# Kernel tuning notes

Measured on AMD Instinct MI355X. Metric: run time of the kernel, lower is better.

Reference implementation:

```python
import jax, jax.numpy as jnp
import numpy as np

DIM = 768
HEADS = 12
HEAD_DIM = DIM // HEADS
SCALE = HEAD_DIM ** (-0.5)


def setup_inputs() -> dict:
    key = jax.random.key(0)
    k1, k2, k3, k4 = jax.random.split(key, 4)
    B, N = 2, 48 * 48
    x = jax.random.normal(k1, (B, N, DIM), dtype=jnp.float32)
    qkv_w = jax.random.normal(k2, (3 * DIM, DIM), dtype=jnp.float32) * (DIM ** -0.5)
    proj_w = jax.random.normal(k3, (DIM, DIM), dtype=jnp.float32) * (DIM ** -0.5)
    proj_b = jax.random.normal(k4, (DIM,), dtype=jnp.float32) * 0.02
    return {"x": x, "H": 48, "W": 48, "qkv_w": qkv_w, "proj_w": proj_w, "proj_b": proj_b}


def reference(x, H, W, qkv_w, proj_w, proj_b):
    B, N, C = x.shape
    h, d = HEADS, HEAD_DIM
    # qkv linear (no bias): [B,N,3C], then split into per-head q,k,v [B,h,N,d]
    qkv = jnp.einsum('bnc,fc->bnf', x, qkv_w)
    qkv = qkv.reshape(B, N, 3, h, d).transpose(2, 0, 3, 1, 4)
    q, k, v = qkv[0], qkv[1], qkv[2]
    attn = jnp.einsum('bhnd,bhmd->bhnm', q, k) * SCALE  # [B,h,N,N]
    attn = jax.nn.softmax(attn, axis=-1)
    out = jnp.einsum('bhnm,bhmd->bhnd', attn, v)  # [B,h,N,d]
    out = out.transpose(0, 2, 1, 3).reshape(B, N, C)
    out = jnp.einsum('bnc,fc->bnf', out, proj_w) + proj_b
    return out
```

## Files before the change

kernel.cpp:

```cpp
#include <hip/hip_runtime.h>

#define B_    2
#define N_    2304
#define C_    768
#define HEADS 12
#define D_    64
#define F3    2304
#define M_    (B_*N_)
#define SPLITS 2
#define KSPAN (N_/SPLITS)
#define QSCALE 0.18033688011112042f

typedef __attribute__((ext_vector_type(8)))  short bfrag;
typedef __attribute__((ext_vector_type(4)))  float ffrag;
typedef __attribute__((ext_vector_type(16))) float ffrag16;

__device__ __forceinline__ short f2bf(float f) {
    unsigned u = __float_as_uint(f);
    u += 0x7fff + ((u >> 16) & 1);
    return (short)(u >> 16);
}

__device__ __forceinline__ void gl2lds16(const void* g, void* l) {
    __builtin_amdgcn_global_load_lds(
        (const __attribute__((address_space(1))) void*)g,
        (__attribute__((address_space(3))) void*)l, 16, 0, 0);
}

__global__ __launch_bounds__(256) void cast_bf16(const float* __restrict__ src,
                                                 short* __restrict__ dst, int n4) {
    int i = blockIdx.x * 256 + threadIdx.x;
    if (i < n4) {
        float4 v = ((const float4*)src)[i];
        short4 o;
        o.x = f2bf(v.x); o.y = f2bf(v.y); o.z = f2bf(v.z); o.w = f2bf(v.w);
        ((short4*)dst)[i] = o;
    }
}

__global__ __launch_bounds__(256) void qkv_gemm(const short* __restrict__ xb,
                                                const short* __restrict__ wb,
                                                short* __restrict__ Qb,
                                                short* __restrict__ Kb,
                                                short* __restrict__ Vtb) {
    __shared__ short As[128*32];
    __shared__ short Bs[128*32];
    const int t = threadIdx.x;
    const int w = t >> 6, lane = t & 63;
    const int quad = lane >> 4, l15 = lane & 15;
    const int wr = w >> 1, wc = w & 1;
    const int m0 = blockIdx.y * 128, f0 = blockIdx.x * 128;

    ffrag acc[4][4] = {};

    for (int k0 = 0; k0 < C_; k0 += 32) {
        __syncthreads();
        #pragma unroll
        for (int r = 0; r < 2; ++r) {
            int seg = r*4 + w;
            int row = seg*16 + (lane >> 2);
            int kk  = (lane & 3) * 8;
            gl2lds16(xb + (size_t)(m0+row)*C_ + k0 + kk, As + seg*512);
            gl2lds16(wb + (size_t)(f0+row)*C_ + k0 + kk, Bs + seg*512);
        }
        __syncthreads();
        bfrag af[4], bf[4];
        #pragma unroll
        for (int i = 0; i < 4; ++i)
            af[i] = *(const bfrag*)(As + (wr*64 + i*16 + l15)*32 + quad*8);
        #pragma unroll
        for (int j = 0; j < 4; ++j)
            bf[j] = *(const bfrag*)(Bs + (wc*64 + j*16 + l15)*32 + quad*8);
        #pragma unroll
        for (int i = 0; i < 4; ++i)
            #pragma unroll
            for (int j = 0; j < 4; ++j)
                acc[i][j] = __builtin_amdgcn_mfma_f32_16x16x32_bf16(af[i], bf[j], acc[i][j], 0, 0, 0);
    }

    const int b   = m0 / N_;
    const int seg = f0 + wc*64;
    const int which = seg / C_;
    const int head  = (seg - which*C_) >> 6;
    const int bh    = b*HEADS + head;
    const int nbase = (m0 - b*N_) + wr*64 + quad*4;

    if (which == 0) {
        #pragma unroll
        for (int i = 0; i < 4; ++i) {
            int n0 = nbase + i*16;
            #pragma unroll
            for (int j = 0; j < 4; ++j) {
                int d = j*16 + l15;
                #pragma unroll
                for (int r = 0; r < 4; ++r)
                    Qb[((size_t)bh*N_ + n0 + r)*D_ + d] = f2bf(acc[i][j][r] * QSCALE);
            }
        }
    } else if (which == 1) {
        #pragma unroll
        for (int i = 0; i < 4; ++i) {
            int n0 = nbase + i*16;
            #pragma unroll
            for (int j = 0; j < 4; ++j) {
                int d = j*16 + l15;
                #pragma unroll
                for (int r = 0; r < 4; ++r)
                    Kb[((size_t)bh*N_ + n0 + r)*D_ + d] = f2bf(acc[i][j][r]);
            }
        }
    } else {
        #pragma unroll
        for (int i = 0; i < 4; ++i) {
            int n0 = nbase + i*16;
            #pragma unroll
            for (int j = 0; j < 4; ++j) {
                int d = j*16 + l15;
                short4 vv;
                vv.x = f2bf(acc[i][j][0]);
                vv.y = f2bf(acc[i][j][1]);
                vv.z = f2bf(acc[i][j][2]);
                vv.w = f2bf(acc[i][j][3]);
                *(short4*)(Vtb + ((size_t)bh*D_ + d)*N_ + n0) = vv;
            }
        }
    }
}

__global__ __launch_bounds__(128) void attn_mfma(const short* __restrict__ Qb,
                                                 const short* __restrict__ Kb,
                                                 const short* __restrict__ Vtb,
                                                 float* __restrict__ Opart,
                                                 float* __restrict__ lpart) {
    __shared__ short PQ[64*72];
    __shared__ short Ks[64*64];
    __shared__ short Vts[64*64];
    const int t = threadIdx.x;
    const int w = t >> 6, lane = t & 63;
    const int l31 = lane & 31, hi = lane >> 5;
    const int bh = blockIdx.x, q0 = blockIdx.y * 64;
    const int split = blockIdx.z;
    const int kbase = split * KSPAN;
    const size_t base = (size_t)bh * N_ * D_;
    const int lrow = lane >> 3;
    const int lc   = (lane & 7) ^ lrow;

    #pragma unroll
    for (int r = 0; r < 4; ++r) {
        int s = r*2 + w;
        int row = s*8 + lrow;
        gl2lds16(Qb + base + (size_t)(q0+row)*D_ + lc*8, PQ + s*512);
    }
    __syncthreads();

    bfrag qf[4];
    {
        int row = w*32 + l31, r7 = row & 7;
        #pragma unroll
        for (int kc = 0; kc < 4; ++kc)
            qf[kc] = *(const bfrag*)(PQ + row*64 + ((kc*2 + hi) ^ r7)*8);
    }

    ffrag16 oacc[2];
    float l_acc[16];
    #pragma unroll
    for (int r = 0; r < 16; ++r) {
        l_acc[r] = 0.f; oacc[0][r] = 0.f; oacc[1][r] = 0.f;
    }

    for (int k0 = kbase; k0 < kbase + KSPAN; k0 += 64) {
        __syncthreads();
        #pragma unroll
        for (int r = 0; r < 4; ++r) {
            int s = r*2 + w;
            int row = s*8 + lrow;
            gl2lds16(Kb  + base + (size_t)(k0+row)*D_ + lc*8,    Ks  + s*512);
            gl2lds16(Vtb + (size_t)(bh*D_ + row)*N_ + k0 + lc*8, Vts + s*512);
        }
        __syncthreads();

        #pragma unroll
        for (int kt = 0; kt < 2; ++kt) {
            ffrag16 s;
            #pragma unroll
            for (int r = 0; r < 16; ++r) s[r] = 0.f;
            int row = kt*32 + l31, r7 = row & 7;
            #pragma unroll
            for (int kc = 0; kc < 4; ++kc) {
                bfrag kf = *(const bfrag*)(Ks + row*64 + ((kc*2 + hi) ^ r7)*8);
                s = __builtin_amdgcn_mfma_f32_32x32x16_bf16(qf[kc], kf, s, 0, 0, 0);
            }
            #pragma unroll
            for (int r = 0; r < 16; ++r) {
                float p = __builtin_amdgcn_exp2f(s[r]);
                l_acc[r] += p;
                int prow = (r & 3) + 8*(r >> 2) + 4*hi;
                PQ[(w*32 + prow)*72 + kt*32 + l31] = f2bf(p);
            }
        }

        #pragma unroll
        for (int kc = 0; kc < 4; ++kc) {
            bfrag pf = *(const bfrag*)(PQ + (w*32 + l31)*72 + kc*16 + hi*8);
            #pragma unroll
            for (int dt = 0; dt < 2; ++dt) {
                int row = dt*32 + l31, r7 = row & 7;
                bfrag vf = *(const bfrag*)(Vts + row*64 + ((kc*2 + hi) ^ r7)*8);
                oacc[dt] = __builtin_amdgcn_mfma_f32_32x32x16_bf16(pf, vf, oacc[dt], 0, 0, 0);
            }
        }
    }

    #pragma unroll
    for (int r = 0; r < 16; ++r) {
        float v = l_acc[r];
        v += __shfl_xor(v, 1, 64);
        v += __shfl_xor(v, 2, 64);
        v += __shfl_xor(v, 4, 64);
        v += __shfl_xor(v, 8, 64);
        v += __shfl_xor(v, 16, 64);
        l_acc[r] = v;
    }

    const int b = bh / HEADS, head = bh - b*HEADS;
    float* Op = Opart + (size_t)split * M_ * C_;
    float* lp = lpart + (size_t)split * (B_*HEADS) * N_;

    if (l31 == 0) {
        #pragma unroll
        for (int r = 0; r < 16; ++r) {
            int n = q0 + w*32 + (r & 3) + 8*(r >> 2) + 4*hi;
            lp[bh*N_ + n] = l_acc[r];
        }
    }
    #pragma unroll
    for (int dt = 0; dt < 2; ++dt)
        #pragma unroll
        for (int r = 0; r < 16; ++r) {
            int n = q0 + w*32 + (r & 3) + 8*(r >> 2) + 4*hi;
            int c = head*D_ + dt*32 + l31;
            Op[((size_t)b*N_ + n)*C_ + c] = oacc[dt][r];
        }
}

__global__ __launch_bounds__(256) void attn_merge(const float* __restrict__ Opart,
                                                  const float* __restrict__ lpart,
                                                  short* __restrict__ Ob) {
    int i = blockIdx.x * 256 + threadIdx.x;
    int m = i / (C_/4);
    int c = (i - m*(C_/4)) * 4;
    int b = m / N_, n = m - b*N_;
    int bh = b*HEADS + (c >> 6);
    float4 o0 = ((const float4*)Opart)[i];
    float4 o1 = ((const float4*)(Opart + (size_t)M_*C_))[i];
    float l = lpart[bh*N_ + n] + lpart[(B_*HEADS)*N_ + bh*N_ + n];
    float inv = 1.f / l;
    short4 o;
    o.x = f2bf((o0.x + o1.x) * inv);
    o.y = f2bf((o0.y + o1.y) * inv);
    o.z = f2bf((o0.z + o1.z) * inv);
    o.w = f2bf((o0.w + o1.w) * inv);
    ((short4*)Ob)[i] = o;
}

__global__ __launch_bounds__(256) void proj_gemm(const short* __restrict__ Ab,
                                                 const short* __restrict__ wb,
                                                 const float* __restrict__ bias,
                                                 float* __restrict__ out) {
    __shared__ short As[128*32];
    __shared__ short Bs[128*32];
    const int t = threadIdx.x;
    const int w = t >> 6, lane = t & 63;
    const int quad = lane >> 4, l15 = lane & 15;
    const int wr = w >> 1, wc = w & 1;
    const int m0 = blockIdx.y * 128, f0 = blockIdx.x * 128;

    ffrag acc[4][4] = {};

    for (int k0 = 0; k0 < C_; k0 += 32) {
        __syncthreads();
        #pragma unroll
        for (int r = 0; r < 2; ++r) {
            int seg = r*4 + w;
            int row = seg*16 + (lane >> 2);
            int kk  = (lane & 3) * 8;
            gl2lds16(Ab + (size_t)(m0+row)*C_ + k0 + kk, As + seg*512);
            gl2lds16(wb + (size_t)(f0+row)*C_ + k0 + kk, Bs + seg*512);
        }
        __syncthreads();
        bfrag af[4], bf[4];
        #pragma unroll
        for (int i = 0; i < 4; ++i)
            af[i] = *(const bfrag*)(As + (wr*64 + i*16 + l15)*32 + quad*8);
        #pragma unroll
        for (int j = 0; j < 4; ++j)
            bf[j] = *(const bfrag*)(Bs + (wc*64 + j*16 + l15)*32 + quad*8);
        #pragma unroll
        for (int i = 0; i < 4; ++i)
            #pragma unroll
            for (int j = 0; j < 4; ++j)
                acc[i][j] = __builtin_amdgcn_mfma_f32_16x16x32_bf16(af[i], bf[j], acc[i][j], 0, 0, 0);
    }

    #pragma unroll
    for (int i = 0; i < 4; ++i) {
        int mbase = m0 + wr*64 + i*16 + quad*4;
        #pragma unroll
        for (int j = 0; j < 4; ++j) {
            int f = f0 + wc*64 + j*16 + l15;
            float bv = bias[f];
            #pragma unroll
            for (int r = 0; r < 4; ++r)
                out[(size_t)(mbase + r)*C_ + f] = acc[i][j][r] + bv;
        }
    }
}

extern "C" void kernel_launch(void* const* d_in, const int* in_sizes, int n_in,
                              void* d_out, int out_size, void* d_ws, size_t ws_size,
                              hipStream_t stream) {
    const float* x      = (const float*)d_in[0];
    const float* qkv_w  = (const float*)d_in[3];
    const float* proj_w = (const float*)d_in[4];
    const float* proj_b = (const float*)d_in[5];
    float* out = (float*)d_out;

    const size_t nx = (size_t)M_ * C_;
    const size_t nq = (size_t)F3 * C_;
    const size_t np = (size_t)C_ * C_;
    short* xb  = (short*)d_ws;
    short* qwb = xb  + nx;
    short* pwb = qwb + nq;
    short* Qb  = pwb + np;
    short* Kb  = Qb  + nx;
    short* Vtb = Kb  + nx;
    short* Ob  = Vtb + nx;
    float* Opart = (float*)(Ob + nx);
    float* lpart = Opart + (size_t)SPLITS * M_ * C_;

    cast_bf16<<<dim3((nx/4 + 255)/256), 256, 0, stream>>>(x,      xb,  (int)(nx/4));
    cast_bf16<<<dim3((nq/4 + 255)/256), 256, 0, stream>>>(qkv_w,  qwb, (int)(nq/4));
    cast_bf16<<<dim3((np/4 + 255)/256), 256, 0, stream>>>(proj_w, pwb, (int)(np/4));

    qkv_gemm<<<dim3(F3/128, M_/128), 256, 0, stream>>>(xb, qwb, Qb, Kb, Vtb);
    attn_mfma<<<dim3(B_*HEADS, N_/64, SPLITS), 128, 0, stream>>>(Qb, Kb, Vtb, Opart, lpart);
    attn_merge<<<dim3((nx/4 + 255)/256), 256, 0, stream>>>(Opart, lpart, Ob);
    proj_gemm<<<dim3(C_/128, M_/128), 256, 0, stream>>>(Ob, pwb, proj_b, out);
}
```

Baseline: 231.7 us.

## Keep softmax probabilities in registers via transposed QK^T MFMA and merge casts

The QK^T MFMA operands are swapped so each lane holds a column of keys for one query. The exponentiated scores are then packed to bf16 and exchanged with a cross-half shuffle, which builds the PV A-operand fragments directly in registers instead of round-tripping through LDS. This removes the LDS stores and loads of P and shrinks the row-sum reduction to a single shuffle. The three cast kernels are also merged into one launch that writes into the contiguous workspace, relying on xb, qwb and pwb being laid out adjacently.

```diff
diff --git a/kernel.cpp b/kernel.cpp
--- a/kernel.cpp
+++ b/kernel.cpp
@@ -14,6 +14,7 @@
 typedef __attribute__((ext_vector_type(8)))  short bfrag;
 typedef __attribute__((ext_vector_type(4)))  float ffrag;
 typedef __attribute__((ext_vector_type(16))) float ffrag16;
+typedef __attribute__((ext_vector_type(4)))  unsigned ufrag;
 
 __device__ __forceinline__ short f2bf(float f) {
     unsigned u = __float_as_uint(f);
@@ -21,21 +22,35 @@
     return (short)(u >> 16);
 }
 
+__device__ __forceinline__ unsigned pk2(float a, float b) {
+    unsigned ua = __float_as_uint(a);
+    ua += 0x7fff + ((ua >> 16) & 1);
+    unsigned ub = __float_as_uint(b);
+    ub += 0x7fff + ((ub >> 16) & 1);
+    return (ua >> 16) | (ub & 0xffff0000u);
+}
+
 __device__ __forceinline__ void gl2lds16(const void* g, void* l) {
     __builtin_amdgcn_global_load_lds(
         (const __attribute__((address_space(1))) void*)g,
         (__attribute__((address_space(3))) void*)l, 16, 0, 0);
 }
 
-__global__ __launch_bounds__(256) void cast_bf16(const float* __restrict__ src,
-                                                 short* __restrict__ dst, int n4) {
+__global__ __launch_bounds__(256) void cast_all(const float* __restrict__ x,
+                                                const float* __restrict__ qw,
+                                                const float* __restrict__ pw,
+                                                short* __restrict__ dst) {
+    const int nx4 = (M_*C_)/4, nq4 = (F3*C_)/4, np4 = (C_*C_)/4;
     int i = blockIdx.x * 256 + threadIdx.x;
-    if (i < n4) {
-        float4 v = ((const float4*)src)[i];
-        short4 o;
-        o.x = f2bf(v.x); o.y = f2bf(v.y); o.z = f2bf(v.z); o.w = f2bf(v.w);
-        ((short4*)dst)[i] = o;
-    }
+    if (i >= nx4 + nq4 + np4) return;
+    const float* src; int off;
+    if (i < nx4)            { src = x;  off = i; }
+    else if (i < nx4 + nq4) { src = qw; off = i - nx4; }
+    else                    { src = pw; off = i - nx4 - nq4; }
+    float4 v = ((const float4*)src)[off];
+    short4 o;
+    o.x = f2bf(v.x); o.y = f2bf(v.y); o.z = f2bf(v.z); o.w = f2bf(v.w);
+    ((short4*)dst)[i] = o;
 }
 
 __global__ __launch_bounds__(256) void qkv_gemm(const short* __restrict__ xb,
@@ -132,7 +147,7 @@
                                                  const short* __restrict__ Vtb,
                                                  float* __restrict__ Opart,
                                                  float* __restrict__ lpart) {
-    __shared__ short PQ[64*72];
+    __shared__ short Qs[64*64];
     __shared__ short Ks[64*64];
     __shared__ short Vts[64*64];
     const int t = threadIdx.x;
@@ -149,7 +164,7 @@
     for (int r = 0; r < 4; ++r) {
         int s = r*2 + w;
         int row = s*8 + lrow;
-        gl2lds16(Qb + base + (size_t)(q0+row)*D_ + lc*8, PQ + s*512);
+        gl2lds16(Qb + base + (size_t)(q0+row)*D_ + lc*8, Qs + s*512);
     }
     __syncthreads();
 
@@ -158,15 +173,13 @@
         int row = w*32 + l31, r7 = row & 7;
         #pragma unroll
         for (int kc = 0; kc < 4; ++kc)
-            qf[kc] = *(const bfrag*)(PQ + row*64 + ((kc*2 + hi) ^ r7)*8);
+            qf[kc] = *(const bfrag*)(Qs + row*64 + ((kc*2 + hi) ^ r7)*8);
     }
 
     ffrag16 oacc[2];
-    float l_acc[16];
     #pragma unroll
-    for (int r = 0; r < 16; ++r) {
-        l_acc[r] = 0.f; oacc[0][r] = 0.f; oacc[1][r] = 0.f;
-    }
+    for (int r = 0; r < 16; ++r) { oacc[0][r] = 0.f; oacc[1][r] = 0.f; }
+    float l_acc = 0.f;
 
     for (int k0 = kbase; k0 < kbase + KSPAN; k0 += 64) {
         __syncthreads();
@@ -179,6 +192,7 @@
         }
         __syncthreads();
 
+        ufrag pfr[4];
         #pragma unroll
         for (int kt = 0; kt < 2; ++kt) {
             ffrag16 s;
@@ -188,20 +202,33 @@
             #pragma unroll
             for (int kc = 0; kc < 4; ++kc) {
                 bfrag kf = *(const bfrag*)(Ks + row*64 + ((kc*2 + hi) ^ r7)*8);
-                s = __builtin_amdgcn_mfma_f32_32x32x16_bf16(qf[kc], kf, s, 0, 0, 0);
+                s = __builtin_amdgcn_mfma_f32_32x32x16_bf16(kf, qf[kc], s, 0, 0, 0);
             }
             #pragma unroll
             for (int r = 0; r < 16; ++r) {
-                float p = __builtin_amdgcn_exp2f(s[r]);
-                l_acc[r] += p;
-                int prow = (r & 3) + 8*(r >> 2) + 4*hi;
-                PQ[(w*32 + prow)*72 + kt*32 + l31] = f2bf(p);
-            }
+                s[r] = __builtin_amdgcn_exp2f(s[r]);
+                l_acc += s[r];
+            }
+            unsigned q01_0 = pk2(s[0],  s[1]),  q23_0 = pk2(s[2],  s[3]);
+            unsigned q01_1 = pk2(s[4],  s[5]),  q23_1 = pk2(s[6],  s[7]);
+            unsigned q01_2 = pk2(s[8],  s[9]),  q23_2 = pk2(s[10], s[11]);
+            unsigned q01_3 = pk2(s[12], s[13]), q23_3 = pk2(s[14], s[15]);
+            unsigned r0 = __shfl_xor(hi ? q01_0 : q01_1, 32, 64);
+            unsigned r1 = __shfl_xor(hi ? q23_0 : q23_1, 32, 64);
+            unsigned r2 = __shfl_xor(hi ? q01_2 : q01_3, 32, 64);
+            unsigned r3 = __shfl_xor(hi ? q23_2 : q23_3, 32, 64);
+            ufrag lo, hif;
+            lo[0] = hi ? r0 : q01_0;  lo[1] = hi ? r1 : q23_0;
+            lo[2] = hi ? q01_1 : r0;  lo[3] = hi ? q23_1 : r1;
+            hif[0] = hi ? r2 : q01_2; hif[1] = hi ? r3 : q23_2;
+            hif[2] = hi ? q01_3 : r2; hif[3] = hi ? q23_3 : r3;
+            pfr[kt*2]     = lo;
+            pfr[kt*2 + 1] = hif;
         }
 
         #pragma unroll
         for (int kc = 0; kc < 4; ++kc) {
-            bfrag pf = *(const bfrag*)(PQ + (w*32 + l31)*72 + kc*16 + hi*8);
+            bfrag pf = __builtin_bit_cast(bfrag, pfr[kc]);
             #pragma unroll
             for (int dt = 0; dt < 2; ++dt) {
                 int row = dt*32 + l31, r7 = row & 7;
@@ -211,28 +238,15 @@
         }
     }
 
-    #pragma unroll
-    for (int r = 0; r < 16; ++r) {
-        float v = l_acc[r];
-        v += __shfl_xor(v, 1, 64);
-        v += __shfl_xor(v, 2, 64);
-        v += __shfl_xor(v, 4, 64);
-        v += __shfl_xor(v, 8, 64);
-        v += __shfl_xor(v, 16, 64);
-        l_acc[r] = v;
-    }
+    l_acc += __shfl_xor(l_acc, 32, 64);
 
     const int b = bh / HEADS, head = bh - b*HEADS;
     float* Op = Opart + (size_t)split * M_ * C_;
     float* lp = lpart + (size_t)split * (B_*HEADS) * N_;
 
-    if (l31 == 0) {
-        #pragma unroll
-        for (int r = 0; r < 16; ++r) {
-            int n = q0 + w*32 + (r & 3) + 8*(r >> 2) + 4*hi;
-            lp[bh*N_ + n] = l_acc[r];
-        }
-    }
+    if (hi == 0)
+        lp[bh*N_ + q0 + w*32 + l31] = l_acc;
+
     #pragma unroll
     for (int dt = 0; dt < 2; ++dt)
         #pragma unroll
@@ -338,12 +352,11 @@
     float* Opart = (float*)(Ob + nx);
     float* lpart = Opart + (size_t)SPLITS * M_ * C_;
 
-    cast_bf16<<<dim3((nx/4 + 255)/256), 256, 0, stream>>>(x,      xb,  (int)(nx/4));
-    cast_bf16<<<dim3((nq/4 + 255)/256), 256, 0, stream>>>(qkv_w,  qwb, (int)(nq/4));
-    cast_bf16<<<dim3((np/4 + 255)/256), 256, 0, stream>>>(proj_w, pwb, (int)(np/4));
+    const int ncast4 = (int)((nx + nq + np) / 4);
+    cast_all<<<dim3((ncast4 + 255)/256), 256, 0, stream>>>(x, qkv_w, proj_w, xb);
 
     qkv_gemm<<<dim3(F3/128, M_/128), 256, 0, stream>>>(xb, qwb, Qb, Kb, Vtb);
     attn_mfma<<<dim3(B_*HEADS, N_/64, SPLITS), 128, 0, stream>>>(Qb, Kb, Vtb, Opart, lpart);
-    attn_merge<<<dim3((nx/4 + 255)/256), 256, 0, stream>>>(Opart, lpart, Ob);
+    attn_merge<<<dim3(((int)(nx/4) + 255)/256), 256, 0, stream>>>(Opart, lpart, Ob);
     proj_gemm<<<dim3(C_/128, M_/128), 256, 0, stream>>>(Ob, pwb, proj_b, out);
 }
```

After: 221.8 us. 1.04x faster.
